# Kernel tuning notes

Hardware: AMD Instinct MI355X
Metric: run time of the kernel (lower is better)

## Reference

```python
import jax, jax.numpy as jnp
import numpy as np

D = 768          # hidden_size
M = 8            # num_patchmerges
B = 16
S = 2048         # non-CLF tokens


def setup_inputs() -> dict:
    key = jax.random.key(0)
    ks = jax.random.split(key, 12)
    std = 0.02
    tokens = jax.random.normal(ks[0], (B, 1 + S, D), dtype=jnp.float32)
    lengths = jnp.maximum(jax.random.randint(ks[1], (B,), 0, S), 1).astype(jnp.int64)
    # PatchMerger: learned queries + layernorm params
    q = jax.random.normal(ks[2], (M, D), dtype=jnp.float32) * std
    ln_scale = jnp.ones((D,), dtype=jnp.float32)
    ln_bias = jnp.zeros((D,), dtype=jnp.float32)
    # mlp1: Linear(3D, D) -> GELU -> Linear(D, D)
    w1a = jax.random.normal(ks[3], (3 * D, D), dtype=jnp.float32) * std
    b1a = jnp.zeros((D,), dtype=jnp.float32)
    w2a = jax.random.normal(ks[4], (D, D), dtype=jnp.float32) * std
    b2a = jnp.zeros((D,), dtype=jnp.float32)
    # mlp2: Linear((1+M)D, D) -> GELU -> Linear(D, D)
    w1b = jax.random.normal(ks[5], ((1 + M) * D, D), dtype=jnp.float32) * std
    b1b = jnp.zeros((D,), dtype=jnp.float32)
    w2b = jax.random.normal(ks[6], (D, D), dtype=jnp.float32) * std
    b2b = jnp.zeros((D,), dtype=jnp.float32)
    return dict(tokens=tokens, lengths=lengths, q=q, ln_scale=ln_scale,
                ln_bias=ln_bias, w1a=w1a, b1a=b1a, w2a=w2a, b2a=b2a,
                w1b=w1b, b1b=b1b, w2b=w2b, b2b=b2b)


def _hpmlp(x, w1, b1, w2, b2):
    h = jax.nn.gelu(x @ w1 + b1, approximate=False)  # dropout=0 -> identity
    return h @ w2 + b2


def _layernorm(x, scale, bias, eps=1e-5):
    mu = jnp.mean(x, axis=-1, keepdims=True)
    var = jnp.var(x, axis=-1, keepdims=True)
    return (x - mu) * jax.lax.rsqrt(var + eps) * scale + bias


def reference(tokens, lengths, q, ln_scale, ln_bias,
              w1a, b1a, w2a, b2a, w1b, b1b, w2b, b2b):
    clf = tokens[:, 0]            # [B, D]
    x = tokens[:, 1:]             # [B, S, D]
    mask = jnp.arange(S)[None, :] < lengths[:, None]   # [B, S]
    mf = mask[..., None].astype(x.dtype)

    # fixed path: masked mean / max / min over valid tokens
    denom = lengths.astype(x.dtype)[:, None]
    mean_p = jnp.sum(x * mf, axis=1) / denom
    max_p = jnp.max(jnp.where(mask[..., None], x, -jnp.inf), axis=1)
    min_p = jnp.min(jnp.where(mask[..., None], x, jnp.inf), axis=1)
    pooled_trad = jnp.concatenate([mean_p, max_p, min_p], axis=-1)  # [B, 3D]
    out_fixed = _hpmlp(pooled_trad, w1a, b1a, w2a, b2a)

    # learned path: PatchMerger (masked attention from M learned queries)
    xn = _layernorm(x, ln_scale, ln_bias)
    scores = jnp.einsum('md,bsd->bms', q, xn) / jnp.sqrt(jnp.asarray(D, x.dtype))
    scores = jnp.where(mask[:, None, :], scores, -jnp.inf)
    attn = jax.nn.softmax(scores, axis=-1)                # [B, M, S]
    merged = jnp.einsum('bms,bsd->bmd', attn, x)          # [B, M, D]
    pooled_learn = jnp.concatenate([merged.reshape(B, M * D), clf], axis=-1)
    out_learn = _hpmlp(pooled_learn, w1b, b1b, w2b, b2b)

    return jnp.concatenate([out_fixed, out_learn], axis=-1)  # [B, 2D]
```

## Files before the change

kernel.cpp:

```cpp
#include <hip/hip_runtime.h>
#include <math.h>

#define SD 768
#define SB 16
#define SM 8
#define SS 2048
#define TOK_ROW 2049
#define NEG_INF (-__builtin_inff())

#define OFF_PPOOL   0
#define OFF_PO      1179648
#define OFF_PML     4325376
#define OFF_PTRAD   4333568
#define OFF_PLEARN  4370432
#define OFF_P1A     4481024
#define OFF_P1B     4591616
#define OFF_HA      4923392
#define OFF_HB      4935680
#define OFF_P2A     4947968
#define OFF_P2B     4984832

__device__ __forceinline__ int clen(int v) { return v < 1 ? 1 : (v > SS ? SS : v); }

__global__ __launch_bounds__(256, 2) void k1_flash(
    const float* __restrict__ tokens, const int* __restrict__ lengths,
    const float* __restrict__ q, const float* __restrict__ lns,
    const float* __restrict__ lnb, float* __restrict__ ppool,
    float* __restrict__ pO, float* __restrict__ pml) {
  int c = blockIdx.x, b = blockIdx.y;
  int len = clen(lengths[b]);
  int c0 = c * 64;
  if (c0 >= len) return;
  int tid = threadIdx.x, w = tid >> 6, lane = tid & 63;
  int mm = lane & 7;

  __shared__ float p_lds[4][16][8];
  __shared__ float pool_lds[4][3][SD];
  __shared__ float O_lds[SM][SD];
  __shared__ float mx_lds[8];

  {
    float* pf = &p_lds[0][0][0];
    for (int i = tid; i < 512; i += 256) pf[i] = NEG_INF;
  }

  float4 qr[8][3];
  float qs1sel, qbsel;
  {
    float4 l4[3], lb4[3];
    #pragma unroll
    for (int g = 0; g < 3; ++g) {
      l4[g] = *(const float4*)(lns + g * 256 + lane * 4);
      lb4[g] = *(const float4*)(lnb + g * 256 + lane * 4);
    }
    float qs1r[8], qbr[8];
    #pragma unroll
    for (int m = 0; m < 8; ++m) {
      float s1 = 0.f, sb = 0.f;
      #pragma unroll
      for (int g = 0; g < 3; ++g) {
        float4 qv = *(const float4*)(q + m * SD + g * 256 + lane * 4);
        float4 qs;
        qs.x = qv.x * l4[g].x; qs.y = qv.y * l4[g].y;
        qs.z = qv.z * l4[g].z; qs.w = qv.w * l4[g].w;
        qr[m][g] = qs;
        s1 += qs.x + qs.y + qs.z + qs.w;
        sb += qv.x * lb4[g].x + qv.y * lb4[g].y + qv.z * lb4[g].z + qv.w * lb4[g].w;
      }
      #pragma unroll
      for (int o = 32; o; o >>= 1) { s1 += __shfl_xor(s1, o, 64); sb += __shfl_xor(sb, o, 64); }
      qs1r[m] = s1; qbr[m] = sb;
    }
    qs1sel = qs1r[0]; qbsel = qbr[0];
    #pragma unroll
    for (int m = 1; m < 8; ++m) {
      qs1sel = (mm == m) ? qs1r[m] : qs1sel;
      qbsel = (mm == m) ? qbr[m] : qbsel;
    }
  }
  __syncthreads();

  float psum[12], pmax[12], pmin[12];
  #pragma unroll
  for (int j = 0; j < 12; ++j) { psum[j] = 0.f; pmax[j] = NEG_INF; pmin[j] = -NEG_INF; }

  int srow = c0 + w * 16;
  int smax = len - srow; if (smax > 16) smax = 16; if (smax < 0) smax = 0;
  const float* xrow = tokens + ((size_t)b * TOK_ROW + 1 + srow) * SD;

  float4 nx0 = {}, nx1 = {}, nx2 = {};
  if (smax > 0) {
    nx0 = *(const float4*)(xrow + lane * 4);
    nx1 = *(const float4*)(xrow + 256 + lane * 4);
    nx2 = *(const float4*)(xrow + 512 + lane * 4);
  }
  for (int i = 0; i < smax; ++i) {
    float4 x0 = nx0, x1 = nx1, x2 = nx2;
    if (i + 1 < smax) {
      const float* xq = xrow + (size_t)(i + 1) * SD;
      nx0 = *(const float4*)(xq + lane * 4);
      nx1 = *(const float4*)(xq + 256 + lane * 4);
      nx2 = *(const float4*)(xq + 512 + lane * 4);
    }
    float xv[12] = {x0.x, x0.y, x0.z, x0.w, x1.x, x1.y, x1.z, x1.w,
                    x2.x, x2.y, x2.z, x2.w};
    float s1 = 0.f, s2 = 0.f;
    #pragma unroll
    for (int j = 0; j < 12; ++j) {
      float v = xv[j];
      psum[j] += v;
      pmax[j] = fmaxf(pmax[j], v);
      pmin[j] = fminf(pmin[j], v);
      s1 += v;
      s2 += v * v;
    }
    float d[8];
    #pragma unroll
    for (int m = 0; m < 8; ++m) {
      float4 a0 = qr[m][0], a1 = qr[m][1], a2 = qr[m][2];
      d[m] = a0.x * xv[0] + a0.y * xv[1] + a0.z * xv[2] + a0.w * xv[3]
           + a1.x * xv[4] + a1.y * xv[5] + a1.z * xv[6] + a1.w * xv[7]
           + a2.x * xv[8] + a2.y * xv[9] + a2.z * xv[10] + a2.w * xv[11];
    }
    #pragma unroll
    for (int o = 1; o <= 4; o <<= 1)
      #pragma unroll
      for (int m = 0; m < 8; ++m) d[m] += __shfl_xor(d[m], o, 64);
    float u = d[0];
    #pragma unroll
    for (int m = 1; m < 8; ++m) u = (mm == m) ? d[m] : u;
    #pragma unroll
    for (int o = 8; o <= 32; o <<= 1) {
      u += __shfl_xor(u, o, 64);
      s1 += __shfl_xor(s1, o, 64);
      s2 += __shfl_xor(s2, o, 64);
    }
    #pragma unroll
    for (int o = 1; o <= 4; o <<= 1) { s1 += __shfl_xor(s1, o, 64); s2 += __shfl_xor(s2, o, 64); }
    float mu = s1 * (1.f / 768.f);
    float var = s2 * (1.f / 768.f) - mu * mu;
    float rstd = rsqrtf(var + 1e-5f);
    float sc = (rstd * u - rstd * mu * qs1sel + qbsel) * 0.03608439182435161f;
    if (lane < 8) p_lds[w][i][lane] = sc;
  }

  #pragma unroll
  for (int g = 0; g < 3; ++g) {
    int dd = g * 256 + lane * 4;
    *(float4*)&pool_lds[w][0][dd] = make_float4(psum[g*4], psum[g*4+1], psum[g*4+2], psum[g*4+3]);
    *(float4*)&pool_lds[w][1][dd] = make_float4(pmax[g*4], pmax[g*4+1], pmax[g*4+2], pmax[g*4+3]);
    *(float4*)&pool_lds[w][2][dd] = make_float4(pmin[g*4], pmin[g*4+1], pmin[g*4+2], pmin[g*4+3]);
  }
  __syncthreads();

  float* pf = &p_lds[0][0][0];
  if (tid < 8) {
    float mxv = NEG_INF;
    for (int r = 0; r < 64; ++r) mxv = fmaxf(mxv, pf[r * 8 + tid]);
    mx_lds[tid] = mxv;
  }
  __syncthreads();
  for (int e = tid; e < 512; e += 256) {
    int m = e & 7;
    pf[e] = __expf(pf[e] - mx_lds[m]);
  }
  __syncthreads();
  if (tid < 8) {
    float lv = 0.f;
    for (int r = 0; r < 64; ++r) lv += pf[r * 8 + tid];
    size_t base = (size_t)(c * SB + b) * 16;
    pml[base + tid] = mx_lds[tid];
    pml[base + 8 + tid] = lv;
  }

  float O[8][12];
  #pragma unroll
  for (int m = 0; m < 8; ++m)
    #pragma unroll
    for (int j = 0; j < 12; ++j) O[m][j] = 0.f;
  if (smax > 0) {
    nx0 = *(const float4*)(xrow + lane * 4);
    nx1 = *(const float4*)(xrow + 256 + lane * 4);
    nx2 = *(const float4*)(xrow + 512 + lane * 4);
  }
  for (int i = 0; i < smax; ++i) {
    float4 x0 = nx0, x1 = nx1, x2 = nx2;
    if (i + 1 < smax) {
      const float* xq = xrow + (size_t)(i + 1) * SD;
      nx0 = *(const float4*)(xq + lane * 4);
      nx1 = *(const float4*)(xq + 256 + lane * 4);
      nx2 = *(const float4*)(xq + 512 + lane * 4);
    }
    float xv[12] = {x0.x, x0.y, x0.z, x0.w, x1.x, x1.y, x1.z, x1.w,
                    x2.x, x2.y, x2.z, x2.w};
    const float4* pr = (const float4*)&p_lds[w][i][0];
    float4 pa = pr[0], pb = pr[1];
    float pm[8] = {pa.x, pa.y, pa.z, pa.w, pb.x, pb.y, pb.z, pb.w};
    #pragma unroll
    for (int m = 0; m < 8; ++m)
      #pragma unroll
      for (int j = 0; j < 12; ++j) O[m][j] += pm[m] * xv[j];
  }
  #pragma unroll
  for (int r = 0; r < 4; ++r) {
    if (w == r) {
      #pragma unroll
      for (int m = 0; m < 8; ++m)
        #pragma unroll
        for (int g = 0; g < 3; ++g) {
          int dd = g * 256 + lane * 4;
          float4 mine = make_float4(O[m][g*4], O[m][g*4+1], O[m][g*4+2], O[m][g*4+3]);
          if (r == 0) {
            *(float4*)&O_lds[m][dd] = mine;
          } else {
            float4 cur = *(float4*)&O_lds[m][dd];
            cur.x += mine.x; cur.y += mine.y; cur.z += mine.z; cur.w += mine.w;
            *(float4*)&O_lds[m][dd] = cur;
          }
        }
    }
    __syncthreads();
  }

  size_t obase = (size_t)(c * SB + b) * 6144;
  const float* of = &O_lds[0][0];
  for (int j = tid * 4; j < 6144; j += 1024)
    *(float4*)&pO[obase + j] = *(const float4*)&of[j];

  size_t pbase = (size_t)(c * SB + b) * 2304;
  for (int j4 = tid * 4; j4 < 2304; j4 += 1024) {
    int stat = j4 / SD, dd = j4 - stat * SD;
    float4 v0 = *(float4*)&pool_lds[0][stat][dd];
    float4 v1 = *(float4*)&pool_lds[1][stat][dd];
    float4 v2 = *(float4*)&pool_lds[2][stat][dd];
    float4 v3 = *(float4*)&pool_lds[3][stat][dd];
    float4 r;
    if (stat == 0) {
      r.x = v0.x + v1.x + v2.x + v3.x; r.y = v0.y + v1.y + v2.y + v3.y;
      r.z = v0.z + v1.z + v2.z + v3.z; r.w = v0.w + v1.w + v2.w + v3.w;
    } else if (stat == 1) {
      r.x = fmaxf(fmaxf(v0.x, v1.x), fmaxf(v2.x, v3.x));
      r.y = fmaxf(fmaxf(v0.y, v1.y), fmaxf(v2.y, v3.y));
      r.z = fmaxf(fmaxf(v0.z, v1.z), fmaxf(v2.z, v3.z));
      r.w = fmaxf(fmaxf(v0.w, v1.w), fmaxf(v2.w, v3.w));
    } else {
      r.x = fminf(fminf(v0.x, v1.x), fminf(v2.x, v3.x));
      r.y = fminf(fminf(v0.y, v1.y), fminf(v2.y, v3.y));
      r.z = fminf(fminf(v0.z, v1.z), fminf(v2.z, v3.z));
      r.w = fminf(fminf(v0.w, v1.w), fminf(v2.w, v3.w));
    }
    *(float4*)&ppool[pbase + j4] = r;
  }
}

__global__ void k_combine(const float* __restrict__ ppool, const float* __restrict__ pO,
                          const float* __restrict__ pml, const float* __restrict__ tokens,
                          const int* __restrict__ lengths,
                          float* __restrict__ ptrad, float* __restrict__ plearn) {
  int tile = blockIdx.x, b = blockIdx.y;
  int len = clen(lengths[b]);
  int nv = (len + 63) >> 6;
  int tid = threadIdx.x;
  __shared__ float pml_lds[32][16];
  __shared__ float e_lds[32][8];
  __shared__ float Linv_lds[8];
  for (int t = tid; t < nv * 16; t += 256) {
    int cc = t >> 4, j = t & 15;
    pml_lds[cc][j] = pml[(size_t)(cc * SB + b) * 16 + j];
  }
  __syncthreads();
  if (tid < 8) {
    float M = NEG_INF;
    for (int cc = 0; cc < nv; ++cc) M = fmaxf(M, pml_lds[cc][tid]);
    float L = 0.f;
    for (int cc = 0; cc < nv; ++cc) {
      float e = __expf(pml_lds[cc][tid] - M);
      e_lds[cc][tid] = e;
      L += e * pml_lds[cc][8 + tid];
    }
    Linv_lds[tid] = 1.f / L;
  }
  __syncthreads();
  #pragma unroll
  for (int k = 0; k < 4; ++k) {
    int jj = tile * 1024 + k * 256 + tid;
    if (jj < 2304) {
      int stat = jj / SD;
      const float* pp = ppool + jj + (size_t)b * 2304;
      if (stat == 0) {
        float a0 = 0.f, a1 = 0.f, a2 = 0.f, a3 = 0.f;
        int cc = 0;
        for (; cc + 4 <= nv; cc += 4) {
          a0 += pp[(size_t)(cc    ) * SB * 2304];
          a1 += pp[(size_t)(cc + 1) * SB * 2304];
          a2 += pp[(size_t)(cc + 2) * SB * 2304];
          a3 += pp[(size_t)(cc + 3) * SB * 2304];
        }
        for (; cc < nv; ++cc) a0 += pp[(size_t)cc * SB * 2304];
        ptrad[b * 2304 + jj] = ((a0 + a1) + (a2 + a3)) / (float)len;
      } else if (stat == 1) {
        float a0 = NEG_INF, a1 = NEG_INF, a2 = NEG_INF, a3 = NEG_INF;
        int cc = 0;
        for (; cc + 4 <= nv; cc += 4) {
          a0 = fmaxf(a0, pp[(size_t)(cc    ) * SB * 2304]);
          a1 = fmaxf(a1, pp[(size_t)(cc + 1) * SB * 2304]);
          a2 = fmaxf(a2, pp[(size_t)(cc + 2) * SB * 2304]);
          a3 = fmaxf(a3, pp[(size_t)(cc + 3) * SB * 2304]);
        }
        for (; cc < nv; ++cc) a0 = fmaxf(a0, pp[(size_t)cc * SB * 2304]);
        ptrad[b * 2304 + jj] = fmaxf(fmaxf(a0, a1), fmaxf(a2, a3));
      } else {
        float a0 = -NEG_INF, a1 = -NEG_INF, a2 = -NEG_INF, a3 = -NEG_INF;
        int cc = 0;
        for (; cc + 4 <= nv; cc += 4) {
          a0 = fminf(a0, pp[(size_t)(cc    ) * SB * 2304]);
          a1 = fminf(a1, pp[(size_t)(cc + 1) * SB * 2304]);
          a2 = fminf(a2, pp[(size_t)(cc + 2) * SB * 2304]);
          a3 = fminf(a3, pp[(size_t)(cc + 3) * SB * 2304]);
        }
        for (; cc < nv; ++cc) a0 = fminf(a0, pp[(size_t)cc * SB * 2304]);
        ptrad[b * 2304 + jj] = fminf(fminf(a0, a1), fminf(a2, a3));
      }
    } else if (jj < 8448) {
      int t = jj - 2304;
      int m = t / SD;
      const float* po = pO + t + (size_t)b * 6144;
      float a0 = 0.f, a1 = 0.f, a2 = 0.f, a3 = 0.f;
      int cc = 0;
      for (; cc + 4 <= nv; cc += 4) {
        a0 += po[(size_t)(cc    ) * SB * 6144] * e_lds[cc    ][m];
        a1 += po[(size_t)(cc + 1) * SB * 6144] * e_lds[cc + 1][m];
        a2 += po[(size_t)(cc + 2) * SB * 6144] * e_lds[cc + 2][m];
        a3 += po[(size_t)(cc + 3) * SB * 6144] * e_lds[cc + 3][m];
      }
      for (; cc < nv; ++cc) a0 += po[(size_t)cc * SB * 6144] * e_lds[cc][m];
      plearn[b * 6912 + t] = ((a0 + a1) + (a2 + a3)) * Linv_lds[m];
    } else {
      int dd = jj - 8448;
      plearn[b * 6912 + 6144 + dd] = tokens[(size_t)b * TOK_ROW * SD + dd];
    }
  }
}

__global__ __launch_bounds__(256) void gemm_partial(
    const float* __restrict__ XA, const float* __restrict__ WA, int ktA, float* __restrict__ PA,
    const float* __restrict__ XB, const float* __restrict__ WB, float* __restrict__ PB) {
  int nt = blockIdx.x, ky = blockIdx.y;
  const float *X, *W; float* P; int kt, ktN;
  if (ky < ktA) { X = XA; W = WA; P = PA; kt = ky; ktN = ktA; }
  else { X = XB; W = WB; P = PB; kt = ky - ktA; ktN = gridDim.y - ktA; }
  int K = ktN * 256;
  int k0 = kt * 256;
  __shared__ __align__(16) float xt[256 * 20];
  __shared__ float red[4][64][17];
  int tid = threadIdx.x;
  #pragma unroll
  for (int b2 = 0; b2 < 16; ++b2) xt[tid * 20 + b2] = X[b2 * K + k0 + tid];
  __syncthreads();
  int w = tid >> 6, lane = tid & 63;
  int n = nt * 64 + lane;
  float acc[16];
  #pragma unroll
  for (int b2 = 0; b2 < 16; ++b2) acc[b2] = 0.f;
  const float* Wp = W + (size_t)k0 * SD + n;
  #pragma unroll 8
  for (int kj = 0; kj < 64; ++kj) {
    int k = w + kj * 4;
    float wv = Wp[(size_t)k * SD];
    const float4* xr = reinterpret_cast<const float4*>(xt + k * 20);
    float4 a0 = xr[0], a1 = xr[1], a2 = xr[2], a3 = xr[3];
    acc[0] += wv * a0.x; acc[1] += wv * a0.y; acc[2] += wv * a0.z; acc[3] += wv * a0.w;
    acc[4] += wv * a1.x; acc[5] += wv * a1.y; acc[6] += wv * a1.z; acc[7] += wv * a1.w;
    acc[8] += wv * a2.x; acc[9] += wv * a2.y; acc[10] += wv * a2.z; acc[11] += wv * a2.w;
    acc[12] += wv * a3.x; acc[13] += wv * a3.y; acc[14] += wv * a3.z; acc[15] += wv * a3.w;
  }
  #pragma unroll
  for (int b2 = 0; b2 < 16; ++b2) red[w][lane][b2] = acc[b2];
  __syncthreads();
  for (int i = tid; i < 1024; i += 256) {
    int nn = i & 63, b2 = i >> 6;
    float r = red[0][nn][b2] + red[1][nn][b2] + red[2][nn][b2] + red[3][nn][b2];
    P[(size_t)(kt * 16 + b2) * SD + nt * 64 + nn] = r;
  }
}

__global__ void gelu_reduce(const float* __restrict__ PA, const float* __restrict__ b1a,
                            float* __restrict__ HA, const float* __restrict__ PB,
                            const float* __restrict__ b1b, float* __restrict__ HB) {
  int y = blockIdx.y;
  int j = blockIdx.x * 256 + threadIdx.x;
  float r;
  if (y == 0) {
    r = b1a[j % SD];
    #pragma unroll
    for (int kt = 0; kt < 9; ++kt) r += PA[kt * 12288 + j];
    HA[j] = r * 0.5f * (1.f + erff(r * 0.70710678118654752f));
  } else {
    r = b1b[j % SD];
    #pragma unroll
    for (int kt = 0; kt < 27; ++kt) r += PB[kt * 12288 + j];
    HB[j] = r * 0.5f * (1.f + erff(r * 0.70710678118654752f));
  }
}

__global__ void final_reduce(const float* __restrict__ P2A, const float* __restrict__ b2a,
                             const float* __restrict__ P2B, const float* __restrict__ b2b,
                             float* __restrict__ out) {
  int y = blockIdx.y;
  const float* P = y ? P2B : P2A;
  const float* bias = y ? b2b : b2a;
  int j = blockIdx.x * 256 + threadIdx.x;
  float r = P[j] + P[12288 + j] + P[24576 + j] + bias[j % SD];
  int b = j / SD, nn = j - b * SD;
  out[b * 1536 + y * SD + nn] = r;
}

extern "C" void kernel_launch(void* const* d_in, const int* in_sizes, int n_in,
                              void* d_out, int out_size, void* d_ws, size_t ws_size,
                              hipStream_t stream) {
  const float* tokens = (const float*)d_in[0];
  const int* lengths  = (const int*)d_in[1];
  const float* q      = (const float*)d_in[2];
  const float* lns    = (const float*)d_in[3];
  const float* lnb    = (const float*)d_in[4];
  const float* w1a    = (const float*)d_in[5];
  const float* b1a    = (const float*)d_in[6];
  const float* w2a    = (const float*)d_in[7];
  const float* b2a    = (const float*)d_in[8];
  const float* w1b    = (const float*)d_in[9];
  const float* b1b    = (const float*)d_in[10];
  const float* w2b    = (const float*)d_in[11];
  const float* b2b    = (const float*)d_in[12];
  float* ws  = (float*)d_ws;
  float* out = (float*)d_out;

  float* ppool  = ws + OFF_PPOOL;
  float* pO     = ws + OFF_PO;
  float* pml    = ws + OFF_PML;
  float* ptrad  = ws + OFF_PTRAD;
  float* plearn = ws + OFF_PLEARN;
  float* p1a    = ws + OFF_P1A;
  float* p1b    = ws + OFF_P1B;
  float* ha     = ws + OFF_HA;
  float* hb     = ws + OFF_HB;
  float* p2a    = ws + OFF_P2A;
  float* p2b    = ws + OFF_P2B;

  k1_flash<<<dim3(32, 16), 256, 0, stream>>>(tokens, lengths, q, lns, lnb, ppool, pO, pml);
  k_combine<<<dim3(9, 16), 256, 0, stream>>>(ppool, pO, pml, tokens, lengths, ptrad, plearn);
  gemm_partial<<<dim3(12, 36), 256, 0, stream>>>(ptrad, w1a, 9, p1a, plearn, w1b, p1b);
  gelu_reduce<<<dim3(48, 2), 256, 0, stream>>>(p1a, b1a, ha, p1b, b1b, hb);
  gemm_partial<<<dim3(12, 6), 256, 0, stream>>>(ha, w2a, 3, p2a, hb, w2b, p2b);
  final_reduce<<<dim3(48, 2), 256, 0, stream>>>(p2a, b2a, p2b, b2b, out);
}
```

Before: 238.9 us.

## Halve GEMM split-K tile, deepen flash prefetch, widen combine unroll

The split-K GEMM tile shrinks from 256 to 128 K-rows, doubling the number of blocks in both MLP GEMMs, and the reduce kernels and workspace offsets are updated to match. The flash kernel's token prefetch goes from one row ahead to two, and the combine loop is unrolled to eight accumulators. The aim is more parallelism in the small GEMMs and more memory-level parallelism when streaming tokens. In exchange there are more partial sums to write and reduce, and more registers in the flash kernel.

```diff
diff --git a/kernel.cpp b/kernel.cpp
--- a/kernel.cpp
+++ b/kernel.cpp
@@ -14,11 +14,11 @@
 #define OFF_PTRAD   4333568
 #define OFF_PLEARN  4370432
 #define OFF_P1A     4481024
-#define OFF_P1B     4591616
-#define OFF_HA      4923392
-#define OFF_HB      4935680
-#define OFF_P2A     4947968
-#define OFF_P2B     4984832
+#define OFF_P1B     4702208
+#define OFF_HA      5365760
+#define OFF_HB      5378048
+#define OFF_P2A     5390336
+#define OFF_P2B     5464064
 
 __device__ __forceinline__ int clen(int v) { return v < 1 ? 1 : (v > SS ? SS : v); }
 
@@ -178,18 +178,26 @@
   for (int m = 0; m < 8; ++m)
     #pragma unroll
     for (int j = 0; j < 12; ++j) O[m][j] = 0.f;
+  float4 a0v = {}, a1v = {}, a2v = {}, b0v = {}, b1v = {}, b2v = {};
   if (smax > 0) {
-    nx0 = *(const float4*)(xrow + lane * 4);
-    nx1 = *(const float4*)(xrow + 256 + lane * 4);
-    nx2 = *(const float4*)(xrow + 512 + lane * 4);
+    a0v = *(const float4*)(xrow + lane * 4);
+    a1v = *(const float4*)(xrow + 256 + lane * 4);
+    a2v = *(const float4*)(xrow + 512 + lane * 4);
+  }
+  if (smax > 1) {
+    const float* xq = xrow + SD;
+    b0v = *(const float4*)(xq + lane * 4);
+    b1v = *(const float4*)(xq + 256 + lane * 4);
+    b2v = *(const float4*)(xq + 512 + lane * 4);
   }
   for (int i = 0; i < smax; ++i) {
-    float4 x0 = nx0, x1 = nx1, x2 = nx2;
-    if (i + 1 < smax) {
-      const float* xq = xrow + (size_t)(i + 1) * SD;
-      nx0 = *(const float4*)(xq + lane * 4);
-      nx1 = *(const float4*)(xq + 256 + lane * 4);
-      nx2 = *(const float4*)(xq + 512 + lane * 4);
+    float4 x0 = a0v, x1 = a1v, x2 = a2v;
+    a0v = b0v; a1v = b1v; a2v = b2v;
+    if (i + 2 < smax) {
+      const float* xq = xrow + (size_t)(i + 2) * SD;
+      b0v = *(const float4*)(xq + lane * 4);
+      b1v = *(const float4*)(xq + 256 + lane * 4);
+      b2v = *(const float4*)(xq + 512 + lane * 4);
     }
     float xv[12] = {x0.x, x0.y, x0.z, x0.w, x1.x, x1.y, x1.z, x1.w,
                     x2.x, x2.y, x2.z, x2.w};
@@ -326,15 +334,20 @@
       int m = t / SD;
       const float* po = pO + t + (size_t)b * 6144;
       float a0 = 0.f, a1 = 0.f, a2 = 0.f, a3 = 0.f;
+      float a4 = 0.f, a5 = 0.f, a6 = 0.f, a7 = 0.f;
       int cc = 0;
-      for (; cc + 4 <= nv; cc += 4) {
+      for (; cc + 8 <= nv; cc += 8) {
         a0 += po[(size_t)(cc    ) * SB * 6144] * e_lds[cc    ][m];
         a1 += po[(size_t)(cc + 1) * SB * 6144] * e_lds[cc + 1][m];
         a2 += po[(size_t)(cc + 2) * SB * 6144] * e_lds[cc + 2][m];
         a3 += po[(size_t)(cc + 3) * SB * 6144] * e_lds[cc + 3][m];
+        a4 += po[(size_t)(cc + 4) * SB * 6144] * e_lds[cc + 4][m];
+        a5 += po[(size_t)(cc + 5) * SB * 6144] * e_lds[cc + 5][m];
+        a6 += po[(size_t)(cc + 6) * SB * 6144] * e_lds[cc + 6][m];
+        a7 += po[(size_t)(cc + 7) * SB * 6144] * e_lds[cc + 7][m];
       }
       for (; cc < nv; ++cc) a0 += po[(size_t)cc * SB * 6144] * e_lds[cc][m];
-      plearn[b * 6912 + t] = ((a0 + a1) + (a2 + a3)) * Linv_lds[m];
+      plearn[b * 6912 + t] = (((a0 + a1) + (a2 + a3)) + ((a4 + a5) + (a6 + a7))) * Linv_lds[m];
     } else {
       int dd = jj - 8448;
       plearn[b * 6912 + 6144 + dd] = tokens[(size_t)b * TOK_ROW * SD + dd];
@@ -349,13 +362,17 @@
   const float *X, *W; float* P; int kt, ktN;
   if (ky < ktA) { X = XA; W = WA; P = PA; kt = ky; ktN = ktA; }
   else { X = XB; W = WB; P = PB; kt = ky - ktA; ktN = gridDim.y - ktA; }
-  int K = ktN * 256;
-  int k0 = kt * 256;
-  __shared__ __align__(16) float xt[256 * 20];
+  int K = ktN * 128;
+  int k0 = kt * 128;
+  __shared__ __align__(16) float xt[128 * 20];
   __shared__ float red[4][64][17];
   int tid = threadIdx.x;
-  #pragma unroll
-  for (int b2 = 0; b2 < 16; ++b2) xt[tid * 20 + b2] = X[b2 * K + k0 + tid];
+  int kk = tid & 127, half = tid >> 7;
+  #pragma unroll
+  for (int u = 0; u < 8; ++u) {
+    int b2 = half * 8 + u;
+    xt[kk * 20 + b2] = X[b2 * K + k0 + kk];
+  }
   __syncthreads();
   int w = tid >> 6, lane = tid & 63;
   int n = nt * 64 + lane;
@@ -364,7 +381,7 @@
   for (int b2 = 0; b2 < 16; ++b2) acc[b2] = 0.f;
   const float* Wp = W + (size_t)k0 * SD + n;
   #pragma unroll 8
-  for (int kj = 0; kj < 64; ++kj) {
+  for (int kj = 0; kj < 32; ++kj) {
     int k = w + kj * 4;
     float wv = Wp[(size_t)k * SD];
     const float4* xr = reinterpret_cast<const float4*>(xt + k * 20);
@@ -393,12 +410,12 @@
   if (y == 0) {
     r = b1a[j % SD];
     #pragma unroll
-    for (int kt = 0; kt < 9; ++kt) r += PA[kt * 12288 + j];
+    for (int kt = 0; kt < 18; ++kt) r += PA[kt * 12288 + j];
     HA[j] = r * 0.5f * (1.f + erff(r * 0.70710678118654752f));
   } else {
     r = b1b[j % SD];
     #pragma unroll
-    for (int kt = 0; kt < 27; ++kt) r += PB[kt * 12288 + j];
+    for (int kt = 0; kt < 54; ++kt) r += PB[kt * 12288 + j];
     HB[j] = r * 0.5f * (1.f + erff(r * 0.70710678118654752f));
   }
 }
@@ -410,7 +427,9 @@
   const float* P = y ? P2B : P2A;
   const float* bias = y ? b2b : b2a;
   int j = blockIdx.x * 256 + threadIdx.x;
-  float r = P[j] + P[12288 + j] + P[24576 + j] + bias[j % SD];
+  float r = bias[j % SD];
+  #pragma unroll
+  for (int kt = 0; kt < 6; ++kt) r += P[kt * 12288 + j];
   int b = j / SD, nn = j - b * SD;
   out[b * 1536 + y * SD + nn] = r;
 }
@@ -448,8 +467,8 @@
 
   k1_flash<<<dim3(32, 16), 256, 0, stream>>>(tokens, lengths, q, lns, lnb, ppool, pO, pml);
   k_combine<<<dim3(9, 16), 256, 0, stream>>>(ppool, pO, pml, tokens, lengths, ptrad, plearn);
-  gemm_partial<<<dim3(12, 36), 256, 0, stream>>>(ptrad, w1a, 9, p1a, plearn, w1b, p1b);
+  gemm_partial<<<dim3(12, 72), 256, 0, stream>>>(ptrad, w1a, 18, p1a, plearn, w1b, p1b);
   gelu_reduce<<<dim3(48, 2), 256, 0, stream>>>(p1a, b1a, ha, p1b, b1b, hb);
-  gemm_partial<<<dim3(12, 6), 256, 0, stream>>>(ha, w2a, 3, p2a, hb, w2b, p2b);
+  gemm_partial<<<dim3(12, 12), 256, 0, stream>>>(ha, w2a, 6, p2a, hb, w2b, p2b);
   final_reduce<<<dim3(48, 2), 256, 0, stream>>>(p2a, b2a, p2b, b2b, out);
 }
```

Measured after the change: 230.6 us. -3.5%, faster.
